# Optimization experiments

Measured on AMD Instinct MI355X. Metric: run time of the kernel, lower is better.

The kernel has to match this reference:

```python
import jax, jax.numpy as jnp
import numpy as np

B, T1, H, P, V = 4096, 65, 64, 50, 32
D = H + P  # input_size = 114


def setup_inputs() -> dict:
    key = jax.random.key(0)
    ks = jax.random.split(key, 20)
    s = 1.0 / np.sqrt(D)
    sh = 1.0 / np.sqrt(H)
    inp = {
        "phonetic_input": jax.random.normal(ks[0], (B, P), dtype=jnp.float32),
        "char_seq": jax.random.randint(ks[1], (B, T1), 0, V, dtype=jnp.int64),
        "emb": jax.random.normal(ks[2], (V, H), dtype=jnp.float32).at[0].set(0.0),  # padding_idx=0
        "W_rx": jax.random.uniform(ks[3], (D, H), jnp.float32, -s, s),
        "b_rx": jax.random.uniform(ks[4], (H,), jnp.float32, -s, s),
        "W_rh": jax.random.uniform(ks[5], (H, H), jnp.float32, -sh, sh),
        "b_rh": jax.random.uniform(ks[6], (H,), jnp.float32, -sh, sh),
        "W_zx": jax.random.uniform(ks[7], (D, H), jnp.float32, -s, s),
        "b_zx": jax.random.uniform(ks[8], (H,), jnp.float32, -s, s),
        "W_zh": jax.random.uniform(ks[9], (H, H), jnp.float32, -sh, sh),
        "b_zh": jax.random.uniform(ks[10], (H,), jnp.float32, -sh, sh),
        "W_hx": jax.random.uniform(ks[11], (D, H), jnp.float32, -s, s),
        "b_hx": jax.random.uniform(ks[12], (H,), jnp.float32, -s, s),
        "W_hh": jax.random.uniform(ks[13], (H, H), jnp.float32, -sh, sh),
        "b_hh": jax.random.uniform(ks[14], (H,), jnp.float32, -sh, sh),
        "W_proj": jax.random.uniform(ks[15], (H, V), jnp.float32, -sh, sh),
        "b_proj": jax.random.uniform(ks[16], (V,), jnp.float32, -sh, sh),
    }
    return inp


def reference(phonetic_input, char_seq, emb, W_rx, b_rx, W_rh, b_rh, W_zx, b_zx,
              W_zh, b_zh, W_hx, b_hx, W_hh, b_hh, W_proj, b_proj):
    input_seq = char_seq[:, :-1]          # [B, T]
    target_seq = char_seq[:, 1:]          # [B, T]
    Bsz, T = input_seq.shape

    char_emb = emb[input_seq]                                   # [B, T, H]
    phon = jnp.broadcast_to(phonetic_input[:, None, :], (Bsz, T, P))
    x = jnp.concatenate([char_emb, phon], axis=2)               # [B, T, D]

    # Hoist input-side projections into batched GEMMs, [T, B, H] for scan
    xr = jnp.einsum('btd,dh->tbh', x, W_rx) + b_rx
    xz = jnp.einsum('btd,dh->tbh', x, W_zx) + b_zx
    xh = jnp.einsum('btd,dh->tbh', x, W_hx) + b_hx

    h0 = jnp.zeros((Bsz, H), dtype=x.dtype)

    def step(h, inputs):
        xr_t, xz_t, xh_t = inputs
        r = jax.nn.sigmoid(xr_t + h @ W_rh + b_rh)
        z = jax.nn.sigmoid(xz_t + h @ W_zh + b_zh)
        c = jnp.tanh(xh_t + (r * h) @ W_hh + b_hh)
        h_new = (1.0 - z) * h + z * c
        return h_new, h_new

    _, hs = jax.lax.scan(step, h0, (xr, xz, xh))                # [T, B, H]
    logits = jnp.einsum('tbh,hv->btv', hs, W_proj) + b_proj     # [B, T, V]

    # cross_entropy with ignore_index=0 (mean over non-ignored)
    targets = target_seq.reshape(-1)
    logp = jax.nn.log_softmax(logits.reshape(-1, V), axis=-1)
    nll = -jnp.take_along_axis(logp, targets[:, None], axis=-1)[:, 0]
    mask = (targets != 0).astype(logits.dtype)
    loss = jnp.sum(nll * mask) / jnp.maximum(jnp.sum(mask), 1.0)
    return logits, loss
```

## Files before the change

kernel.cpp:

```cpp
#include <hip/hip_runtime.h>
#include <stdint.h>

#define Bsz 4096
#define Tn  64
#define T1n 65
#define Hn  64
#define Pn  50
#define Vn  32

typedef __attribute__((ext_vector_type(8))) short short8;
typedef __attribute__((ext_vector_type(4))) unsigned short bf16x4;
typedef __attribute__((ext_vector_type(4))) float floatx4;

__device__ __forceinline__ float bf2f(unsigned short u) {
  union { unsigned int i; float f; } x; x.i = ((unsigned int)u) << 16; return x.f;
}
__device__ __forceinline__ unsigned short f2bf(float f) {
  union { float f; unsigned int i; } x; x.f = f;
  return (unsigned short)((x.i + 0x7FFFu + ((x.i >> 16) & 1u)) >> 16);
}
__device__ __forceinline__ unsigned int packbf(float a, float b) {
  return (unsigned int)f2bf(a) | ((unsigned int)f2bf(b) << 16);
}
__device__ __forceinline__ float fast_sigmoid(float x) {
  return __builtin_amdgcn_rcpf(1.f + __expf(-x));
}
__device__ __forceinline__ float fast_tanh(float x) {
  return 1.f - 2.f * __builtin_amdgcn_rcpf(1.f + __expf(2.f * x));
}
__device__ __forceinline__ void bar_lgkm() {
  asm volatile("s_waitcnt lgkmcnt(0)\n\ts_barrier" ::: "memory");
}

__device__ __forceinline__ short8 load_bfrag(const float* __restrict__ W, int ncols, int col, int kbase) {
  short8 f;
#pragma unroll
  for (int j = 0; j < 8; ++j) f[j] = (short)f2bf(W[(long)(kbase + j) * ncols + col]);
  return f;
}

__launch_bounds__(512)
__global__ void gru_kernel(const float* __restrict__ phon,
                           const int* __restrict__ cs,
                           const float* __restrict__ emb,
                           const float* __restrict__ Wrx, const float* __restrict__ brx,
                           const float* __restrict__ Wrh, const float* __restrict__ brh,
                           const float* __restrict__ Wzx, const float* __restrict__ bzx,
                           const float* __restrict__ Wzh, const float* __restrict__ bzh,
                           const float* __restrict__ Whx, const float* __restrict__ bhx,
                           const float* __restrict__ Whh, const float* __restrict__ bhh,
                           const float* __restrict__ Wpj, const float* __restrict__ bpj_g,
                           float* __restrict__ ws,
                           float* __restrict__ outp) {
  __shared__ __align__(16) unsigned short tbl_s[3 * 32 * 68];
  __shared__ __align__(16) unsigned int hp_s[16 * 36];
  __shared__ __align__(16) unsigned int rhp_s[16 * 36];
  __shared__ unsigned char codes_s[66 * 16];
  __shared__ float sum_s[2 * 16];
  __shared__ float tl_s[16];
  __shared__ int det_s[1];

  const int tid = threadIdx.x;
  const int b0 = blockIdx.x * 16;
  const int W8 = tid >> 6, lane = tid & 63, q = lane >> 4, c16 = lane & 15;
  const floatx4 zf = {0.f, 0.f, 0.f, 0.f};

  if (tid == 0) det_s[0] = 0;
  __syncthreads();
  if (tid < 128 && cs[2 * tid + 1] != 0) atomicOr(&det_s[0], 1);
  __syncthreads();
  const bool is64 = (det_s[0] == 0);

  for (int i = tid; i < 16 * 36; i += 512) hp_s[i] = 0;
  for (int i = tid; i < 65 * 16; i += 512) {
    int t = i >> 4, b = i & 15;
    long idx = (long)(b0 + b) * T1n + t;
    int c = is64 ? cs[2 * idx] : cs[idx];
    codes_s[i] = (unsigned char)(c & 255);
  }

  for (int g = 0; g < 3; ++g) {
    const float* Wg = (g == 0) ? Wrx : (g == 1) ? Wzx : Whx;
    const float* bx = (g == 0) ? brx : (g == 1) ? bzx : bhx;
    const float* bh = (g == 0) ? brh : (g == 1) ? bzh : bhh;
    float acc[4] = {0.f, 0.f, 0.f, 0.f};
    float bias = bx[lane] + bh[lane];
    for (int d = 0; d < Hn; ++d) {
      float wv = Wg[(long)d * Hn + lane];
#pragma unroll
      for (int k = 0; k < 4; ++k)
        acc[k] += emb[(long)(W8 + 8 * k) * Hn + d] * wv;
    }
#pragma unroll
    for (int k = 0; k < 4; ++k)
      tbl_s[g * 2176 + (W8 + 8 * k) * 68 + lane] = f2bf(acc[k] + bias);
  }

  const bool isGate = (W8 < 4);
  const bool isProj = (W8 == 4 || W8 == 5);
  const int w = W8 & 3;
  const int m = W8 - 4;
  const int tb = 16 * w + 4 * q;

  short8 zs = {0,0,0,0,0,0,0,0};
  short8 Ar0 = zs, Ar1 = zs, Az0 = zs, Az1 = zs, Ah0 = zs, Ah1 = zs;
  short8 Ap0 = zs, Ap1 = zs;
  float ph_r[4] = {0,0,0,0}, ph_z[4] = {0,0,0,0}, ph_h[4] = {0,0,0,0};
  float bpjr[4] = {0,0,0,0};
  if (isGate) {
    Ar0 = load_bfrag(Wrh, Hn, 16 * w + c16, 8 * q);
    Ar1 = load_bfrag(Wrh, Hn, 16 * w + c16, 32 + 8 * q);
    Az0 = load_bfrag(Wzh, Hn, 16 * w + c16, 8 * q);
    Az1 = load_bfrag(Wzh, Hn, 16 * w + c16, 32 + 8 * q);
    Ah0 = load_bfrag(Whh, Hn, 16 * w + c16, 8 * q);
    Ah1 = load_bfrag(Whh, Hn, 16 * w + c16, 32 + 8 * q);
    for (int p = 0; p < Pn; ++p) {
      float xv = phon[(long)(b0 + c16) * Pn + p];
      floatx4 wr = *(const floatx4*)&Wrx[(long)(Hn + p) * Hn + tb];
      floatx4 wz = *(const floatx4*)&Wzx[(long)(Hn + p) * Hn + tb];
      floatx4 wh = *(const floatx4*)&Whx[(long)(Hn + p) * Hn + tb];
#pragma unroll
      for (int reg = 0; reg < 4; ++reg) {
        ph_r[reg] += xv * wr[reg];
        ph_z[reg] += xv * wz[reg];
        ph_h[reg] += xv * wh[reg];
      }
    }
  } else if (isProj) {
    Ap0 = load_bfrag(Wpj, Vn, 16 * m + c16, 8 * q);
    Ap1 = load_bfrag(Wpj, Vn, 16 * m + c16, 32 + 8 * q);
#pragma unroll
    for (int reg = 0; reg < 4; ++reg) bpjr[reg] = bpj_g[16 * m + 4 * q + reg];
  }

  const int hp_rd = c16 * 36 + 4 * q;
  const int hp_wr = c16 * 36 + 8 * w + 2 * q;

  float h4[4] = {0.f, 0.f, 0.f, 0.f};
  float z4[4] = {0.f, 0.f, 0.f, 0.f};
  float nll = 0.f, cnt = 0.f;
  int code = 0;
  floatx4 lacc = zf;

  __syncthreads();

  for (int t = 0; t <= Tn + 1; ++t) {
    if (isGate) {
      if (t < Tn) {
        code = codes_s[t * 16 + c16];
        short8 hb0 = *(const short8*)&hp_s[hp_rd];
        short8 hb1 = *(const short8*)&hp_s[hp_rd + 16];
        floatx4 accr = __builtin_amdgcn_mfma_f32_16x16x32_bf16(Ar0, hb0, zf, 0, 0, 0);
        floatx4 accz = __builtin_amdgcn_mfma_f32_16x16x32_bf16(Az0, hb0, zf, 0, 0, 0);
        accr = __builtin_amdgcn_mfma_f32_16x16x32_bf16(Ar1, hb1, accr, 0, 0, 0);
        accz = __builtin_amdgcn_mfma_f32_16x16x32_bf16(Az1, hb1, accz, 0, 0, 0);
        bf16x4 tvr = *(const bf16x4*)&tbl_s[code * 68 + tb];
        bf16x4 tvz = *(const bf16x4*)&tbl_s[2176 + code * 68 + tb];
        float rh[4];
#pragma unroll
        for (int reg = 0; reg < 4; ++reg) {
          float xr = bf2f(tvr[reg]) + ph_r[reg] + accr[reg];
          float xz = bf2f(tvz[reg]) + ph_z[reg] + accz[reg];
          z4[reg] = fast_sigmoid(xz);
          rh[reg] = fast_sigmoid(xr) * h4[reg];
        }
        unsigned long long wv = (unsigned long long)packbf(rh[0], rh[1])
                              | ((unsigned long long)packbf(rh[2], rh[3]) << 32);
        *(unsigned long long*)&rhp_s[hp_wr] = wv;
      }
    } else if (isProj) {
      if (t >= 1 && t <= Tn) {
        short8 hb0 = *(const short8*)&hp_s[hp_rd];
        short8 hb1 = *(const short8*)&hp_s[hp_rd + 16];
        lacc = __builtin_amdgcn_mfma_f32_16x16x32_bf16(Ap0, hb0, zf, 0, 0, 0);
        lacc = __builtin_amdgcn_mfma_f32_16x16x32_bf16(Ap1, hb1, lacc, 0, 0, 0);
      }
    } else if (W8 == 6) {
      if (t >= 2 && lane < 16) {
        int targ = codes_s[(t - 1) * 16 + lane];
        if (targ != 0) {
          float s = sum_s[lane] + sum_s[16 + lane];
          nll += __logf(s) - tl_s[lane];
          cnt += 1.f;
        }
      }
    }
    bar_lgkm();

    if (isGate) {
      if (t < Tn) {
        short8 p0 = *(const short8*)&rhp_s[hp_rd];
        short8 p1 = *(const short8*)&rhp_s[hp_rd + 16];
        floatx4 acch = __builtin_amdgcn_mfma_f32_16x16x32_bf16(Ah0, p0, zf, 0, 0, 0);
        acch = __builtin_amdgcn_mfma_f32_16x16x32_bf16(Ah1, p1, acch, 0, 0, 0);
        bf16x4 tvh = *(const bf16x4*)&tbl_s[4352 + code * 68 + tb];
#pragma unroll
        for (int reg = 0; reg < 4; ++reg) {
          float xh = bf2f(tvh[reg]) + ph_h[reg] + acch[reg];
          float c = fast_tanh(xh);
          h4[reg] = fmaf(z4[reg], c - h4[reg], h4[reg]);
        }
        unsigned long long wv = (unsigned long long)packbf(h4[0], h4[1])
                              | ((unsigned long long)packbf(h4[2], h4[3]) << 32);
        *(unsigned long long*)&hp_s[hp_wr] = wv;
      }
    } else if (isProj) {
      if (t >= 1 && t <= Tn) {
        const int p = t - 1;
        float lg[4]; float e = 0.f;
#pragma unroll
        for (int reg = 0; reg < 4; ++reg) {
          lg[reg] = lacc[reg] + bpjr[reg];
          e += __expf(lg[reg]);
        }
        e += __shfl_xor(e, 16);
        e += __shfl_xor(e, 32);
        if (q == 0) sum_s[m * 16 + c16] = e;
        int targ = codes_s[t * 16 + c16];
#pragma unroll
        for (int reg = 0; reg < 4; ++reg)
          if (targ != 0 && targ == 16 * m + 4 * q + reg) tl_s[c16] = lg[reg];
        floatx4 st = {lg[0], lg[1], lg[2], lg[3]};
        *(floatx4*)&outp[((long)(b0 + c16) * Tn + p) * Vn + 16 * m + 4 * q] = st;
      }
    }
    bar_lgkm();
  }

  if (W8 == 6) {
#pragma unroll
    for (int off = 8; off >= 1; off >>= 1) {
      nll += __shfl_xor(nll, off);
      cnt += __shfl_xor(cnt, off);
    }
    if (lane == 0) {
      ws[2 * blockIdx.x] = nll;
      ws[2 * blockIdx.x + 1] = cnt;
    }
  }
}

__global__ void loss_kernel(const float* __restrict__ ws, float* __restrict__ outp) {
  int lane = threadIdx.x;
  float n = 0.f, c = 0.f;
  for (int i = lane; i < Bsz / 16; i += 64) { n += ws[2 * i]; c += ws[2 * i + 1]; }
#pragma unroll
  for (int off = 32; off >= 1; off >>= 1) {
    n += __shfl_xor(n, off);
    c += __shfl_xor(c, off);
  }
  if (lane == 0) outp[(size_t)Bsz * Tn * Vn] = n / fmaxf(c, 1.f);
}

extern "C" void kernel_launch(void* const* d_in, const int* in_sizes, int n_in,
                              void* d_out, int out_size, void* d_ws, size_t ws_size,
                              hipStream_t stream) {
  const float* phon = (const float*)d_in[0];
  const int*   cs   = (const int*)d_in[1];
  const float* emb  = (const float*)d_in[2];
  const float* Wrx  = (const float*)d_in[3];
  const float* brx  = (const float*)d_in[4];
  const float* Wrh  = (const float*)d_in[5];
  const float* brh  = (const float*)d_in[6];
  const float* Wzx  = (const float*)d_in[7];
  const float* bzx  = (const float*)d_in[8];
  const float* Wzh  = (const float*)d_in[9];
  const float* bzh  = (const float*)d_in[10];
  const float* Whx  = (const float*)d_in[11];
  const float* bhx  = (const float*)d_in[12];
  const float* Whh  = (const float*)d_in[13];
  const float* bhh  = (const float*)d_in[14];
  const float* Wpj  = (const float*)d_in[15];
  const float* bpj  = (const float*)d_in[16];
  float* ws = (float*)d_ws;

  hipLaunchKernelGGL(gru_kernel, dim3(Bsz / 16), dim3(512), 0, stream,
                     phon, cs, emb, Wrx, brx, Wrh, brh, Wzx, bzx, Wzh, bzh,
                     Whx, bhx, Whh, bhh, Wpj, bpj, ws, (float*)d_out);
  hipLaunchKernelGGL(loss_kernel, dim3(1), dim3(64), 0, stream, ws, (float*)d_out);
}
```

Baseline: 176.8 us.

## Split GRU gates across dedicated waves with double-buffered hidden state

Raises the block from 8 to 15 waves and gives each recurrent matmul its own group of four waves: r-gate, z-gate and candidate/h-update. Hidden state and z now pass between waves through shared memory, and the bf16 hidden buffer is double-buffered. The projection waves read the previous h in the second phase, so each step's serial chain per wave gets shorter. In exchange the block needs more threads and LDS, fewer blocks fit per CU, and the extra fp32 state exchanges add LDS traffic.

```diff
diff --git a/kernel.cpp b/kernel.cpp
--- a/kernel.cpp
+++ b/kernel.cpp
@@ -8,6 +8,9 @@
 #define Pn  50
 #define Vn  32
 
+#define NWAVE 15
+#define NT    960
+
 typedef __attribute__((ext_vector_type(8))) short short8;
 typedef __attribute__((ext_vector_type(4))) unsigned short bf16x4;
 typedef __attribute__((ext_vector_type(4))) float floatx4;
@@ -39,7 +42,7 @@
   return f;
 }
 
-__launch_bounds__(512)
+__launch_bounds__(NT)
 __global__ void gru_kernel(const float* __restrict__ phon,
                            const int* __restrict__ cs,
                            const float* __restrict__ emb,
@@ -53,11 +56,13 @@
                            float* __restrict__ ws,
                            float* __restrict__ outp) {
   __shared__ __align__(16) unsigned short tbl_s[3 * 32 * 68];
-  __shared__ __align__(16) unsigned int hp_s[16 * 36];
-  __shared__ __align__(16) unsigned int rhp_s[16 * 36];
+  __shared__ __align__(16) unsigned int hK_s[2][16 * 36];
+  __shared__ __align__(16) unsigned int rhK_s[16 * 36];
+  __shared__ __align__(16) float zC_s[4][16 * 20];
+  __shared__ __align__(16) float hC_s[4][16 * 20];
   __shared__ unsigned char codes_s[66 * 16];
-  __shared__ float sum_s[2 * 16];
-  __shared__ float tl_s[16];
+  __shared__ float sum_s[2][2][16];
+  __shared__ float tl_s[2][16];
   __shared__ int det_s[1];
 
   const int tid = threadIdx.x;
@@ -71,8 +76,9 @@
   __syncthreads();
   const bool is64 = (det_s[0] == 0);
 
-  for (int i = tid; i < 16 * 36; i += 512) hp_s[i] = 0;
-  for (int i = tid; i < 65 * 16; i += 512) {
+  for (int i = tid; i < 16 * 36; i += NT) hK_s[1][i] = 0;
+  for (int i = tid; i < 4 * 16 * 20; i += NT) ((float*)hC_s)[i] = 0.f;
+  for (int i = tid; i < 65 * 16; i += NT) {
     int t = i >> 4, b = i & 15;
     long idx = (long)(b0 + b) * T1n + t;
     int c = is64 ? cs[2 * idx] : cs[idx];
@@ -83,129 +89,134 @@
     const float* Wg = (g == 0) ? Wrx : (g == 1) ? Wzx : Whx;
     const float* bx = (g == 0) ? brx : (g == 1) ? bzx : bhx;
     const float* bh = (g == 0) ? brh : (g == 1) ? bzh : bhh;
-    float acc[4] = {0.f, 0.f, 0.f, 0.f};
+    float acc[3] = {0.f, 0.f, 0.f};
     float bias = bx[lane] + bh[lane];
     for (int d = 0; d < Hn; ++d) {
       float wv = Wg[(long)d * Hn + lane];
 #pragma unroll
-      for (int k = 0; k < 4; ++k)
-        acc[k] += emb[(long)(W8 + 8 * k) * Hn + d] * wv;
-    }
-#pragma unroll
-    for (int k = 0; k < 4; ++k)
-      tbl_s[g * 2176 + (W8 + 8 * k) * 68 + lane] = f2bf(acc[k] + bias);
-  }
-
-  const bool isGate = (W8 < 4);
-  const bool isProj = (W8 == 4 || W8 == 5);
-  const int w = W8 & 3;
-  const int m = W8 - 4;
-  const int tb = 16 * w + 4 * q;
+      for (int k = 0; k < 3; ++k) {
+        int v = W8 + NWAVE * k;
+        if (v < 32) acc[k] += emb[(long)v * Hn + d] * wv;
+      }
+    }
+#pragma unroll
+    for (int k = 0; k < 3; ++k) {
+      int v = W8 + NWAVE * k;
+      if (v < 32) tbl_s[g * 2176 + v * 68 + lane] = f2bf(acc[k] + bias);
+    }
+  }
+
+  const int role = (W8 < 4) ? 0 : (W8 < 8) ? 1 : (W8 < 12) ? 2 : (W8 < 14) ? 3 : 4;
+  const int u = W8 & 3;
+  const int m = W8 - 12;
+  const int tb = 16 * u + 4 * q;
 
   short8 zs = {0,0,0,0,0,0,0,0};
-  short8 Ar0 = zs, Ar1 = zs, Az0 = zs, Az1 = zs, Ah0 = zs, Ah1 = zs;
-  short8 Ap0 = zs, Ap1 = zs;
-  float ph_r[4] = {0,0,0,0}, ph_z[4] = {0,0,0,0}, ph_h[4] = {0,0,0,0};
-  float bpjr[4] = {0,0,0,0};
-  if (isGate) {
-    Ar0 = load_bfrag(Wrh, Hn, 16 * w + c16, 8 * q);
-    Ar1 = load_bfrag(Wrh, Hn, 16 * w + c16, 32 + 8 * q);
-    Az0 = load_bfrag(Wzh, Hn, 16 * w + c16, 8 * q);
-    Az1 = load_bfrag(Wzh, Hn, 16 * w + c16, 32 + 8 * q);
-    Ah0 = load_bfrag(Whh, Hn, 16 * w + c16, 8 * q);
-    Ah1 = load_bfrag(Whh, Hn, 16 * w + c16, 32 + 8 * q);
+  short8 A0 = zs, A1 = zs;
+  float ph[4] = {0.f, 0.f, 0.f, 0.f};
+  float bpjr[4] = {0.f, 0.f, 0.f, 0.f};
+  if (role == 0) {
+    A0 = load_bfrag(Wrh, Hn, 16 * u + c16, 8 * q);
+    A1 = load_bfrag(Wrh, Hn, 16 * u + c16, 32 + 8 * q);
+  } else if (role == 1) {
+    A0 = load_bfrag(Wzh, Hn, 16 * u + c16, 8 * q);
+    A1 = load_bfrag(Wzh, Hn, 16 * u + c16, 32 + 8 * q);
+  } else if (role == 2) {
+    A0 = load_bfrag(Whh, Hn, 16 * u + c16, 8 * q);
+    A1 = load_bfrag(Whh, Hn, 16 * u + c16, 32 + 8 * q);
+  } else if (role == 3) {
+    A0 = load_bfrag(Wpj, Vn, 16 * m + c16, 8 * q);
+    A1 = load_bfrag(Wpj, Vn, 16 * m + c16, 32 + 8 * q);
+#pragma unroll
+    for (int reg = 0; reg < 4; ++reg) bpjr[reg] = bpj_g[16 * m + 4 * q + reg];
+  }
+  if (role < 3) {
+    const float* Wg = (role == 0) ? Wrx : (role == 1) ? Wzx : Whx;
     for (int p = 0; p < Pn; ++p) {
       float xv = phon[(long)(b0 + c16) * Pn + p];
-      floatx4 wr = *(const floatx4*)&Wrx[(long)(Hn + p) * Hn + tb];
-      floatx4 wz = *(const floatx4*)&Wzx[(long)(Hn + p) * Hn + tb];
-      floatx4 wh = *(const floatx4*)&Whx[(long)(Hn + p) * Hn + tb];
-#pragma unroll
-      for (int reg = 0; reg < 4; ++reg) {
-        ph_r[reg] += xv * wr[reg];
-        ph_z[reg] += xv * wz[reg];
-        ph_h[reg] += xv * wh[reg];
-      }
-    }
-  } else if (isProj) {
-    Ap0 = load_bfrag(Wpj, Vn, 16 * m + c16, 8 * q);
-    Ap1 = load_bfrag(Wpj, Vn, 16 * m + c16, 32 + 8 * q);
-#pragma unroll
-    for (int reg = 0; reg < 4; ++reg) bpjr[reg] = bpj_g[16 * m + 4 * q + reg];
+      floatx4 w4 = *(const floatx4*)&Wg[(long)(Hn + p) * Hn + tb];
+#pragma unroll
+      for (int reg = 0; reg < 4; ++reg) ph[reg] += xv * w4[reg];
+    }
   }
 
   const int hp_rd = c16 * 36 + 4 * q;
-  const int hp_wr = c16 * 36 + 8 * w + 2 * q;
+  const int hp_wr = c16 * 36 + 8 * u + 2 * q;
+  const int cC    = c16 * 20 + 4 * q;
 
   float h4[4] = {0.f, 0.f, 0.f, 0.f};
-  float z4[4] = {0.f, 0.f, 0.f, 0.f};
   float nll = 0.f, cnt = 0.f;
-  int code = 0;
-  floatx4 lacc = zf;
 
   __syncthreads();
 
   for (int t = 0; t <= Tn + 1; ++t) {
-    if (isGate) {
+    if (role == 0) {
       if (t < Tn) {
-        code = codes_s[t * 16 + c16];
-        short8 hb0 = *(const short8*)&hp_s[hp_rd];
-        short8 hb1 = *(const short8*)&hp_s[hp_rd + 16];
-        floatx4 accr = __builtin_amdgcn_mfma_f32_16x16x32_bf16(Ar0, hb0, zf, 0, 0, 0);
-        floatx4 accz = __builtin_amdgcn_mfma_f32_16x16x32_bf16(Az0, hb0, zf, 0, 0, 0);
-        accr = __builtin_amdgcn_mfma_f32_16x16x32_bf16(Ar1, hb1, accr, 0, 0, 0);
-        accz = __builtin_amdgcn_mfma_f32_16x16x32_bf16(Az1, hb1, accz, 0, 0, 0);
-        bf16x4 tvr = *(const bf16x4*)&tbl_s[code * 68 + tb];
-        bf16x4 tvz = *(const bf16x4*)&tbl_s[2176 + code * 68 + tb];
+        int code = codes_s[t * 16 + c16];
+        const unsigned int* hp = hK_s[(t + 1) & 1];
+        short8 hb0 = *(const short8*)&hp[hp_rd];
+        short8 hb1 = *(const short8*)&hp[hp_rd + 16];
+        floatx4 hc = *(const floatx4*)&hC_s[u][cC];
+        floatx4 acc = __builtin_amdgcn_mfma_f32_16x16x32_bf16(A0, hb0, zf, 0, 0, 0);
+        acc = __builtin_amdgcn_mfma_f32_16x16x32_bf16(A1, hb1, acc, 0, 0, 0);
+        bf16x4 tv = *(const bf16x4*)&tbl_s[code * 68 + tb];
         float rh[4];
 #pragma unroll
         for (int reg = 0; reg < 4; ++reg) {
-          float xr = bf2f(tvr[reg]) + ph_r[reg] + accr[reg];
-          float xz = bf2f(tvz[reg]) + ph_z[reg] + accz[reg];
-          z4[reg] = fast_sigmoid(xz);
-          rh[reg] = fast_sigmoid(xr) * h4[reg];
+          float xr = bf2f(tv[reg]) + ph[reg] + acc[reg];
+          rh[reg] = fast_sigmoid(xr) * hc[reg];
         }
         unsigned long long wv = (unsigned long long)packbf(rh[0], rh[1])
                               | ((unsigned long long)packbf(rh[2], rh[3]) << 32);
-        *(unsigned long long*)&rhp_s[hp_wr] = wv;
-      }
-    } else if (isProj) {
-      if (t >= 1 && t <= Tn) {
-        short8 hb0 = *(const short8*)&hp_s[hp_rd];
-        short8 hb1 = *(const short8*)&hp_s[hp_rd + 16];
-        lacc = __builtin_amdgcn_mfma_f32_16x16x32_bf16(Ap0, hb0, zf, 0, 0, 0);
-        lacc = __builtin_amdgcn_mfma_f32_16x16x32_bf16(Ap1, hb1, lacc, 0, 0, 0);
-      }
-    } else if (W8 == 6) {
-      if (t >= 2 && lane < 16) {
-        int targ = codes_s[(t - 1) * 16 + lane];
-        if (targ != 0) {
-          float s = sum_s[lane] + sum_s[16 + lane];
-          nll += __logf(s) - tl_s[lane];
-          cnt += 1.f;
-        }
+        *(unsigned long long*)&rhK_s[hp_wr] = wv;
+      }
+    } else if (role == 1) {
+      if (t < Tn) {
+        int code = codes_s[t * 16 + c16];
+        const unsigned int* hp = hK_s[(t + 1) & 1];
+        short8 hb0 = *(const short8*)&hp[hp_rd];
+        short8 hb1 = *(const short8*)&hp[hp_rd + 16];
+        floatx4 acc = __builtin_amdgcn_mfma_f32_16x16x32_bf16(A0, hb0, zf, 0, 0, 0);
+        acc = __builtin_amdgcn_mfma_f32_16x16x32_bf16(A1, hb1, acc, 0, 0, 0);
+        bf16x4 tv = *(const bf16x4*)&tbl_s[2176 + code * 68 + tb];
+        floatx4 z4;
+#pragma unroll
+        for (int reg = 0; reg < 4; ++reg) {
+          float xz = bf2f(tv[reg]) + ph[reg] + acc[reg];
+          z4[reg] = fast_sigmoid(xz);
+        }
+        *(floatx4*)&zC_s[u][cC] = z4;
       }
     }
     bar_lgkm();
 
-    if (isGate) {
+    if (role == 2) {
       if (t < Tn) {
-        short8 p0 = *(const short8*)&rhp_s[hp_rd];
-        short8 p1 = *(const short8*)&rhp_s[hp_rd + 16];
-        floatx4 acch = __builtin_amdgcn_mfma_f32_16x16x32_bf16(Ah0, p0, zf, 0, 0, 0);
-        acch = __builtin_amdgcn_mfma_f32_16x16x32_bf16(Ah1, p1, acch, 0, 0, 0);
-        bf16x4 tvh = *(const bf16x4*)&tbl_s[4352 + code * 68 + tb];
+        int code = codes_s[t * 16 + c16];
+        short8 p0 = *(const short8*)&rhK_s[hp_rd];
+        short8 p1 = *(const short8*)&rhK_s[hp_rd + 16];
+        floatx4 acc = __builtin_amdgcn_mfma_f32_16x16x32_bf16(A0, p0, zf, 0, 0, 0);
+        acc = __builtin_amdgcn_mfma_f32_16x16x32_bf16(A1, p1, acc, 0, 0, 0);
+        bf16x4 tv = *(const bf16x4*)&tbl_s[4352 + code * 68 + tb];
+        floatx4 z4 = *(const floatx4*)&zC_s[u][cC];
 #pragma unroll
         for (int reg = 0; reg < 4; ++reg) {
-          float xh = bf2f(tvh[reg]) + ph_h[reg] + acch[reg];
+          float xh = bf2f(tv[reg]) + ph[reg] + acc[reg];
           float c = fast_tanh(xh);
           h4[reg] = fmaf(z4[reg], c - h4[reg], h4[reg]);
         }
+        *(floatx4*)&hC_s[u][cC] = *(const floatx4*)h4;
         unsigned long long wv = (unsigned long long)packbf(h4[0], h4[1])
                               | ((unsigned long long)packbf(h4[2], h4[3]) << 32);
-        *(unsigned long long*)&hp_s[hp_wr] = wv;
-      }
-    } else if (isProj) {
+        *(unsigned long long*)&hK_s[t & 1][hp_wr] = wv;
+      }
+    } else if (role == 3) {
       if (t >= 1 && t <= Tn) {
+        const unsigned int* hp = hK_s[(t + 1) & 1];
+        short8 hb0 = *(const short8*)&hp[hp_rd];
+        short8 hb1 = *(const short8*)&hp[hp_rd + 16];
+        floatx4 lacc = __builtin_amdgcn_mfma_f32_16x16x32_bf16(A0, hb0, zf, 0, 0, 0);
+        lacc = __builtin_amdgcn_mfma_f32_16x16x32_bf16(A1, hb1, lacc, 0, 0, 0);
         const int p = t - 1;
         float lg[4]; float e = 0.f;
 #pragma unroll
@@ -215,19 +226,29 @@
         }
         e += __shfl_xor(e, 16);
         e += __shfl_xor(e, 32);
-        if (q == 0) sum_s[m * 16 + c16] = e;
+        if (q == 0) sum_s[t & 1][m][c16] = e;
         int targ = codes_s[t * 16 + c16];
 #pragma unroll
         for (int reg = 0; reg < 4; ++reg)
-          if (targ != 0 && targ == 16 * m + 4 * q + reg) tl_s[c16] = lg[reg];
+          if (targ != 0 && targ == 16 * m + 4 * q + reg) tl_s[t & 1][c16] = lg[reg];
         floatx4 st = {lg[0], lg[1], lg[2], lg[3]};
         *(floatx4*)&outp[((long)(b0 + c16) * Tn + p) * Vn + 16 * m + 4 * q] = st;
       }
+    } else if (role == 4) {
+      if (t >= 2 && t <= Tn + 1 && lane < 16) {
+        int targ = codes_s[(t - 1) * 16 + lane];
+        if (targ != 0) {
+          int sl = (t - 1) & 1;
+          float s = sum_s[sl][0][lane] + sum_s[sl][1][lane];
+          nll += __logf(s) - tl_s[sl][lane];
+          cnt += 1.f;
+        }
+      }
     }
     bar_lgkm();
   }
 
-  if (W8 == 6) {
+  if (role == 4) {
 #pragma unroll
     for (int off = 8; off >= 1; off >>= 1) {
       nll += __shfl_xor(nll, off);
@@ -274,7 +295,7 @@
   const float* bpj  = (const float*)d_in[16];
   float* ws = (float*)d_ws;
 
-  hipLaunchKernelGGL(gru_kernel, dim3(Bsz / 16), dim3(512), 0, stream,
+  hipLaunchKernelGGL(gru_kernel, dim3(Bsz / 16), dim3(NT), 0, stream,
                      phon, cs, emb, Wrx, brx, Wrh, brh, Wzx, bzx, Wzh, bzh,
                      Whx, bhx, Whh, bhh, Wpj, bpj, ws, (float*)d_out);
   hipLaunchKernelGGL(loss_kernel, dim3(1), dim3(64), 0, stream, ws, (float*)d_out);
```

Result: slower. 220.8 us (+24.9%).
